# Kernel optimization log

Measured on AMD Instinct MI355X. Metric: run time of the kernel, lower is better.

Reference implementation:

```python
import jax, jax.numpy as jnp
import numpy as np

ALPHA = 4
N_NODES = 100000
N_EDGES = 1600000
DIM = 128


def setup_inputs() -> dict:
    key = jax.random.key(0)
    ks = jax.random.split(key, 7)
    x = jax.random.normal(ks[0], (N_NODES, DIM), dtype=jnp.float32)
    edge_index = jax.random.randint(ks[1], (ALPHA, 2, N_EDGES), 0, N_NODES, dtype=jnp.int64)
    edge_attr = jax.random.uniform(ks[2], (ALPHA, N_EDGES), dtype=jnp.float32)
    lin_w = jax.random.normal(ks[3], (DIM, DIM), dtype=jnp.float32) * 0.05
    lin_b = jax.random.normal(ks[4], (DIM,), dtype=jnp.float32) * 0.05
    conv_w = jax.random.normal(ks[5], (ALPHA, DIM, DIM), dtype=jnp.float32) * 0.05
    conv_b = jax.random.normal(ks[6], (ALPHA, DIM), dtype=jnp.float32) * 0.05
    return {"x": x, "edge_index": edge_index, "edge_attr": edge_attr,
            "lin_w": lin_w, "lin_b": lin_b, "conv_w": conv_w, "conv_b": conv_b}


def _gcn_conv(h, row, col, w, weight, bias):
    # gcn_norm with add_self_loops=False
    deg = jax.ops.segment_sum(w, col, num_segments=N_NODES)          # [N]
    dinv = jnp.where(deg > 0, jax.lax.rsqrt(deg), 0.0)               # deg^{-1/2}
    norm = dinv[row] * w * dinv[col]                                 # [E]
    hw = h @ weight.T                                                # [N, D] (Linear(in,out))
    msg = norm[:, None] * hw[row]                                    # gather + scale, [E, D]
    out = jax.ops.segment_sum(msg, col, num_segments=N_NODES)        # scatter-add, [N, D]
    return out + bias


def reference(x, edge_index, edge_attr, lin_w, lin_b, conv_w, conv_b):
    # dropout is identity in eval mode (training=False)
    h = jax.nn.relu(x @ lin_w.T + lin_b)
    hs = [h]
    for i in range(ALPHA):
        row, col = edge_index[i, 0], edge_index[i, 1]
        h = _gcn_conv(hs[-1], row, col, edge_attr[i], conv_w[i], conv_b[i])
        h = jax.nn.relu(h)
        hs.append(h)
    return jnp.stack(hs)  # [ALPHA+1, N, D] (torch returns list of these)
```

## Files before the change

### kernel.cpp

```cpp
#include <hip/hip_runtime.h>

#define NN 100000
#define NE 1600000
#define DD 128
#define SCAN_CHUNK 1024
#define NBLK ((NN + SCAN_CHUNK - 1) / SCAN_CHUNK)

using u16 = unsigned short;
using u32 = unsigned int;
using u64 = unsigned long long;

typedef __bf16 bf16x8 __attribute__((ext_vector_type(8)));
typedef float  f32x4  __attribute__((ext_vector_type(4)));

__device__ __forceinline__ float bf2f(u16 h){ return __uint_as_float(((u32)h) << 16); }
__device__ __forceinline__ u16 f2bf(float f){
  u32 u = __float_as_uint(f);
  u += 0x7FFFu + ((u >> 16) & 1u);
  return (u16)(u >> 16);
}
__device__ __forceinline__ int ld_idx(const int* __restrict__ p, long long k, int w64){
  return w64 ? p[2*k] : p[k];
}
__device__ __forceinline__ float ldf(const void* __restrict__ p, long long k, int f32){
  return f32 ? ((const float*)p)[k] : bf2f(((const u16*)p)[k]);
}

__global__ void detect_kernel(const int* __restrict__ ei, const u16* __restrict__ xw,
                              int* __restrict__ flags){
  if (threadIdx.x == 0 && blockIdx.x == 0){
    int all0 = 1;
    for (int k = 1; k < 256; k += 2) all0 &= (ei[k] == 0);
    flags[0] = all0;
    int cnt = 0;
    for (int i = 0; i < 128; ++i){
      u16 w = xw[2*i];
      int e = (w >> 7) & 0xFF;
      cnt += (e >= 100 && e <= 130);
    }
    flags[1] = (cnt < 64);
  }
}

__global__ __launch_bounds__(256) void prep_w_kernel(const void* __restrict__ lin_w,
    const void* __restrict__ conv_w, const int* __restrict__ flags, u16* __restrict__ wbf){
  int i = blockIdx.x*256 + threadIdx.x;
  if (i >= 5*DD*DD) return;
  int f32 = flags[1];
  float v = (i < DD*DD) ? ldf(lin_w, i, f32) : ldf(conv_w, i - DD*DD, f32);
  wbf[i] = f2bf(v);
}

__global__ __launch_bounds__(256) void hist_kernel(const void* __restrict__ ea, long long ea_off,
    const int* __restrict__ ei, long long col_off,
    const int* __restrict__ flags, u64* __restrict__ pk){
  int e = blockIdx.x*256 + threadIdx.x;
  if (e >= NE) return;
  int col = ld_idx(ei, col_off + e, flags[0]);
  float w = ldf(ea, ea_off + e, flags[1]);
  u64 v = (1ull << 40) | (u64)(w * 16777216.0f);
  atomicAdd(pk + col, v);
}

__global__ __launch_bounds__(256) void dinv_kernel(const u64* __restrict__ pk,
    float* __restrict__ dinv, int* __restrict__ cnt){
  int n = blockIdx.x*256 + threadIdx.x;
  if (n >= NN) return;
  u64 p = pk[n];
  cnt[n] = (int)(p >> 40);
  float d = (float)(p & ((1ull << 40) - 1)) * (1.0f/16777216.0f);
  dinv[n] = (d > 0.f) ? rsqrtf(d) : 0.f;
}

__global__ __launch_bounds__(256) void scan_block_kernel(const int* __restrict__ cnt,
    int* __restrict__ base, int* __restrict__ bsums){
  __shared__ int sm[256];
  int b = blockIdx.x, t = threadIdx.x;
  int i0 = b*SCAN_CHUNK + t*4;
  int v[4];
  #pragma unroll
  for (int j = 0; j < 4; ++j) v[j] = (i0 + j < NN) ? cnt[i0 + j] : 0;
  int s = v[0] + v[1] + v[2] + v[3];
  sm[t] = s;
  __syncthreads();
  for (int off = 1; off < 256; off <<= 1){
    int add = (t >= off) ? sm[t - off] : 0;
    __syncthreads();
    sm[t] += add;
    __syncthreads();
  }
  int run = sm[t] - s;
  if (t == 255) bsums[b] = sm[255];
  #pragma unroll
  for (int j = 0; j < 4; ++j){
    if (i0 + j < NN) base[i0 + j] = run;
    run += v[j];
  }
}

__global__ void scan_sums_kernel(int* __restrict__ bsums, int nb){
  __shared__ int sm[256];
  int t = threadIdx.x;
  int v = (t < nb) ? bsums[t] : 0;
  sm[t] = v;
  __syncthreads();
  for (int off = 1; off < 256; off <<= 1){
    int add = (t >= off) ? sm[t - off] : 0;
    __syncthreads();
    sm[t] += add;
    __syncthreads();
  }
  if (t < nb) bsums[t] = sm[t] - v;
}

__global__ __launch_bounds__(256) void scan_add_kernel(int* __restrict__ base,
    const int* __restrict__ bsums, int* __restrict__ cursor){
  int i = blockIdx.x*256 + threadIdx.x;
  if (i >= NN) return;
  int b = base[i] + bsums[i / SCAN_CHUNK];
  base[i] = b;
  cursor[i] = b;
}

__global__ __launch_bounds__(256) void fill_kernel(const void* __restrict__ ea, long long ea_off,
    const int* __restrict__ ei, long long row_off, long long col_off,
    const float* __restrict__ dinv, const int* __restrict__ flags,
    int* __restrict__ cursor, int2* __restrict__ rc){
  int e = blockIdx.x*256 + threadIdx.x;
  if (e >= NE) return;
  int w64 = flags[0];
  int row = ld_idx(ei, row_off + e, w64);
  int col = ld_idx(ei, col_off + e, w64);
  float w = ldf(ea, ea_off + e, flags[1]);
  int pos = atomicAdd(cursor + col, 1);
  rc[pos] = make_int2(row, __float_as_int(dinv[row] * w * dinv[col]));
}

__global__ __launch_bounds__(256) void aggregate_kernel(
    const void* __restrict__ hbase, long long h_off,
    const int2* __restrict__ rc,
    const int* __restrict__ base, const int* __restrict__ cnt,
    const int* __restrict__ flags, void* __restrict__ agg, int agg_f32){
  int wid = (int)(((long long)blockIdx.x*256 + threadIdx.x) >> 6);
  int l = threadIdx.x & 63;
  if (wid >= NN) return;
  int f32 = flags[1];
  int s = base[wid], e = s + cnt[wid];
  float ax = 0.f, ay = 0.f;

  if (f32){
    const float2* hp = (const float2*)((const float*)hbase + h_off);
    int j = s;
    for (; j + 8 <= e; j += 8){
      int2 v[8];
      #pragma unroll
      for (int k = 0; k < 8; ++k) v[k] = rc[j + k];
      float2 hv[8];
      #pragma unroll
      for (int k = 0; k < 8; ++k) hv[k] = hp[(long long)v[k].x*64 + l];
      #pragma unroll
      for (int k = 0; k < 8; ++k){
        float c = __int_as_float(v[k].y);
        ax += c*hv[k].x; ay += c*hv[k].y;
      }
    }
    if (j < e){
      int2 v[8];
      #pragma unroll
      for (int k = 0; k < 8; ++k){
        int jj = (j + k < e) ? (j + k) : s;
        v[k] = rc[jj];
        if (j + k >= e) v[k].y = 0;
      }
      float2 hv[8];
      #pragma unroll
      for (int k = 0; k < 8; ++k) hv[k] = hp[(long long)v[k].x*64 + l];
      #pragma unroll
      for (int k = 0; k < 8; ++k){
        float c = __int_as_float(v[k].y);
        ax += c*hv[k].x; ay += c*hv[k].y;
      }
    }
  } else {
    const u32* hp = (const u32*)((const u16*)hbase + h_off);
    int j = s;
    for (; j + 8 <= e; j += 8){
      int2 v[8];
      #pragma unroll
      for (int k = 0; k < 8; ++k) v[k] = rc[j + k];
      u32 hv[8];
      #pragma unroll
      for (int k = 0; k < 8; ++k) hv[k] = hp[(long long)v[k].x*64 + l];
      #pragma unroll
      for (int k = 0; k < 8; ++k){
        float c = __int_as_float(v[k].y);
        ax += c*bf2f((u16)(hv[k] & 0xFFFF));
        ay += c*bf2f((u16)(hv[k] >> 16));
      }
    }
    if (j < e){
      int2 v[8];
      #pragma unroll
      for (int k = 0; k < 8; ++k){
        int jj = (j + k < e) ? (j + k) : s;
        v[k] = rc[jj];
        if (j + k >= e) v[k].y = 0;
      }
      u32 hv[8];
      #pragma unroll
      for (int k = 0; k < 8; ++k) hv[k] = hp[(long long)v[k].x*64 + l];
      #pragma unroll
      for (int k = 0; k < 8; ++k){
        float c = __int_as_float(v[k].y);
        ax += c*bf2f((u16)(hv[k] & 0xFFFF));
        ay += c*bf2f((u16)(hv[k] >> 16));
      }
    }
  }
  if (agg_f32) ((float2*)agg)[(long long)wid*64 + l] = make_float2(ax, ay);
  else         ((u32*)agg)[(long long)wid*64 + l] = ((u32)f2bf(ay) << 16) | (u32)f2bf(ax);
}

__global__ __launch_bounds__(256) void gemm_mfma_kernel(
    const void* __restrict__ in, int in_mode,
    const u16* __restrict__ wbf,
    const void* __restrict__ bias, long long b_off,
    const int* __restrict__ flags,
    void* __restrict__ outb, long long out_off){
  __shared__ u16 ah[64*DD];
  __shared__ u16 al[64*DD];
  int t = threadIdx.x;
  int f32 = flags[1];
  int inf32 = (in_mode == 2) ? f32 : in_mode;
  long long rowbase = (long long)blockIdx.x * 64;

  #pragma unroll
  for (int it = 0; it < 8; ++it){
    int i = (it*256 + t) * 4;
    int r = i >> 7, c = i & 127;
    long long gr = rowbase + r;
    float v0, v1, v2, v3;
    if (gr < NN){
      if (inf32){
        const float4 f = *(const float4*)((const float*)in + gr*DD + c);
        v0 = f.x; v1 = f.y; v2 = f.z; v3 = f.w;
      } else {
        const ushort4 u = *(const ushort4*)((const u16*)in + gr*DD + c);
        v0 = bf2f(u.x); v1 = bf2f(u.y); v2 = bf2f(u.z); v3 = bf2f(u.w);
      }
    } else { v0 = v1 = v2 = v3 = 0.f; }
    u16 h0 = f2bf(v0), h1 = f2bf(v1), h2 = f2bf(v2), h3 = f2bf(v3);
    u16 l0 = f2bf(v0 - bf2f(h0)), l1 = f2bf(v1 - bf2f(h1));
    u16 l2 = f2bf(v2 - bf2f(h2)), l3 = f2bf(v3 - bf2f(h3));
    int idx = (r*DD + c) ^ ((r & 7) << 3);
    *(ushort4*)&ah[idx] = make_ushort4(h0, h1, h2, h3);
    *(ushort4*)&al[idx] = make_ushort4(l0, l1, l2, l3);
  }
  __syncthreads();

  const int w  = t >> 6, l = t & 63;
  const int lr = l & 15, lg = l >> 4;
  const int arow = w*16 + lr;
  f32x4 acc[8];
  #pragma unroll
  for (int j = 0; j < 8; ++j) acc[j] = (f32x4){0.f, 0.f, 0.f, 0.f};

  #pragma unroll
  for (int s = 0; s < 4; ++s){
    const int kb = s*32 + lg*8;
    const int aidx = (arow*DD + kb) ^ ((arow & 7) << 3);
    bf16x8 afh = *(const bf16x8*)&ah[aidx];
    bf16x8 afl = *(const bf16x8*)&al[aidx];
    #pragma unroll
    for (int tt = 0; tt < 8; ++tt){
      bf16x8 bfr = *(const bf16x8*)&wbf[(tt*16 + lr)*DD + kb];
      acc[tt] = __builtin_amdgcn_mfma_f32_16x16x32_bf16(afh, bfr, acc[tt], 0, 0, 0);
      acc[tt] = __builtin_amdgcn_mfma_f32_16x16x32_bf16(afl, bfr, acc[tt], 0, 0, 0);
    }
  }

  const long long gn0 = rowbase + w*16 + lg*4;
  #pragma unroll
  for (int tt = 0; tt < 8; ++tt){
    const int d = tt*16 + lr;
    const float bv = ldf(bias, b_off + d, f32);
    #pragma unroll
    for (int q = 0; q < 4; ++q){
      long long gn = gn0 + q;
      if (gn < NN){
        float vv = fmaxf(acc[tt][q] + bv, 0.f);
        long long gi = out_off + gn*DD + d;
        if (f32) ((float*)outb)[gi] = vv;
        else     ((u16*)outb)[gi] = f2bf(vv);
      }
    }
  }
}

extern "C" void kernel_launch(void* const* d_in, const int* in_sizes, int n_in,
                              void* d_out, int out_size, void* d_ws, size_t ws_size,
                              hipStream_t stream){
  const void* x      = d_in[0];
  const int*  ei     = (const int*)d_in[1];
  const void* ea     = d_in[2];
  const void* lin_w  = d_in[3];
  const void* lin_b  = d_in[4];
  const void* conv_w = d_in[5];
  const void* conv_b = d_in[6];
  void* out = d_out;

  char* ws = (char*)d_ws;
  size_t o = 0;
  auto alloc = [&](size_t bytes){ void* p = ws + o; o = (o + bytes + 255) & ~(size_t)255; return p; };
  int*   flags  = (int*)  alloc(256);
  u64*   pk     = (u64*)  alloc((size_t)NN*8);
  float* dinv   = (float*)alloc((size_t)NN*4);
  int*   cnt    = (int*)  alloc((size_t)NN*4);
  int*   base   = (int*)  alloc((size_t)NN*4);
  int*   cursor = (int*)  alloc((size_t)NN*4);
  int*   bsums  = (int*)  alloc(4096);
  int2*  rc     = (int2*) alloc((size_t)NE*8);
  u16*   wbf    = (u16*)  alloc((size_t)5*DD*DD*2);
  size_t fixed = o;
  int agg_f32 = (ws_size >= fixed + (size_t)NN*DD*4) ? 1 : 0;
  void* agg = alloc((size_t)NN*DD*(agg_f32 ? 4 : 2));

  detect_kernel<<<1, 64, 0, stream>>>(ei, (const u16*)x, flags);
  prep_w_kernel<<<(5*DD*DD + 255)/256, 256, 0, stream>>>(lin_w, conv_w, flags, wbf);

  gemm_mfma_kernel<<<(NN+63)/64, 256, 0, stream>>>(x, 2, wbf, lin_b, 0, flags, out, 0);

  for (int i = 0; i < 4; ++i){
    long long h_off   = (long long)i*NN*DD;
    long long o_off   = (long long)(i+1)*NN*DD;
    long long row_off = ((long long)i*2 + 0)*NE;
    long long col_off = ((long long)i*2 + 1)*NE;
    long long ea_off  = (long long)i*NE;

    hipMemsetAsync(pk, 0, (size_t)NN*8, stream);
    hist_kernel<<<(NE+255)/256, 256, 0, stream>>>(ea, ea_off, ei, col_off, flags, pk);
    dinv_kernel<<<(NN+255)/256, 256, 0, stream>>>(pk, dinv, cnt);

    scan_block_kernel<<<NBLK, 256, 0, stream>>>(cnt, base, bsums);
    scan_sums_kernel<<<1, 256, 0, stream>>>(bsums, NBLK);
    scan_add_kernel<<<(NN+255)/256, 256, 0, stream>>>(base, bsums, cursor);

    fill_kernel<<<(NE+255)/256, 256, 0, stream>>>(ea, ea_off, ei, row_off, col_off,
                                                  dinv, flags, cursor, rc);

    aggregate_kernel<<<(NN*64 + 255)/256, 256, 0, stream>>>(out, h_off, rc,
                                                            base, cnt, flags, agg, agg_f32);

    gemm_mfma_kernel<<<(NN+63)/64, 256, 0, stream>>>(agg, agg_f32 ? 1 : 0,
                                                     wbf + (size_t)(1+i)*DD*DD,
                                                     conv_b, (long long)i*DD, flags, out, o_off);
  }
}
```

Before: 1.624 ms.

## Batch CSR build across layers and fuse aggregation with MFMA GEMM

The per-layer histogram, scan and fill kernels become single launches that cover all four layers, using padded per-layer arrays. The aggregation is fused into the GEMM: each block gathers 64 node rows into shared memory as a split hi/lo bf16 pair and multiplies them with MFMA directly, so the intermediate agg buffer is never written to or read from global memory. In exchange, each block now does 64 rows of irregular gather before its GEMM, which may lower parallelism during the gather phase, and the CSR workspace grows fourfold.

```diff
diff --git a/kernel.cpp b/kernel.cpp
--- a/kernel.cpp
+++ b/kernel.cpp
@@ -5,6 +5,9 @@
 #define DD 128
 #define SCAN_CHUNK 1024
 #define NBLK ((NN + SCAN_CHUNK - 1) / SCAN_CHUNK)
+#define NNP (NBLK * SCAN_CHUNK)
+#define NTOT (4 * NNP)
+#define BPL ((NE + 255) / 256)
 
 using u16 = unsigned short;
 using u32 = unsigned int;
@@ -51,21 +54,23 @@
   wbf[i] = f2bf(v);
 }
 
-__global__ __launch_bounds__(256) void hist_kernel(const void* __restrict__ ea, long long ea_off,
-    const int* __restrict__ ei, long long col_off,
-    const int* __restrict__ flags, u64* __restrict__ pk){
-  int e = blockIdx.x*256 + threadIdx.x;
+__global__ __launch_bounds__(256) void hist_all_kernel(const void* __restrict__ ea,
+    const int* __restrict__ ei, const int* __restrict__ flags, u64* __restrict__ pk){
+  int lyr = blockIdx.x / BPL;
+  int e = (blockIdx.x - lyr*BPL)*256 + threadIdx.x;
   if (e >= NE) return;
+  long long col_off = ((long long)lyr*2 + 1)*NE;
+  long long ea_off  = (long long)lyr*NE;
   int col = ld_idx(ei, col_off + e, flags[0]);
   float w = ldf(ea, ea_off + e, flags[1]);
   u64 v = (1ull << 40) | (u64)(w * 16777216.0f);
-  atomicAdd(pk + col, v);
-}
-
-__global__ __launch_bounds__(256) void dinv_kernel(const u64* __restrict__ pk,
+  atomicAdd(pk + (size_t)lyr*NNP + col, v);
+}
+
+__global__ __launch_bounds__(256) void dinv_all_kernel(const u64* __restrict__ pk,
     float* __restrict__ dinv, int* __restrict__ cnt){
   int n = blockIdx.x*256 + threadIdx.x;
-  if (n >= NN) return;
+  if (n >= NTOT) return;
   u64 p = pk[n];
   cnt[n] = (int)(p >> 40);
   float d = (float)(p & ((1ull << 40) - 1)) * (1.0f/16777216.0f);
@@ -79,7 +84,7 @@
   int i0 = b*SCAN_CHUNK + t*4;
   int v[4];
   #pragma unroll
-  for (int j = 0; j < 4; ++j) v[j] = (i0 + j < NN) ? cnt[i0 + j] : 0;
+  for (int j = 0; j < 4; ++j) v[j] = cnt[i0 + j];
   int s = v[0] + v[1] + v[2] + v[3];
   sm[t] = s;
   __syncthreads();
@@ -93,7 +98,7 @@
   if (t == 255) bsums[b] = sm[255];
   #pragma unroll
   for (int j = 0; j < 4; ++j){
-    if (i0 + j < NN) base[i0 + j] = run;
+    base[i0 + j] = run;
     run += v[j];
   }
 }
@@ -101,7 +106,8 @@
 __global__ void scan_sums_kernel(int* __restrict__ bsums, int nb){
   __shared__ int sm[256];
   int t = threadIdx.x;
-  int v = (t < nb) ? bsums[t] : 0;
+  int* bs = bsums + blockIdx.x*nb;
+  int v = (t < nb) ? bs[t] : 0;
   sm[t] = v;
   __syncthreads();
   for (int off = 1; off < 256; off <<= 1){
@@ -110,115 +116,34 @@
     sm[t] += add;
     __syncthreads();
   }
-  if (t < nb) bsums[t] = sm[t] - v;
+  if (t < nb) bs[t] = sm[t] - v;
 }
 
 __global__ __launch_bounds__(256) void scan_add_kernel(int* __restrict__ base,
     const int* __restrict__ bsums, int* __restrict__ cursor){
   int i = blockIdx.x*256 + threadIdx.x;
-  if (i >= NN) return;
+  if (i >= NTOT) return;
   int b = base[i] + bsums[i / SCAN_CHUNK];
   base[i] = b;
   cursor[i] = b;
 }
 
-__global__ __launch_bounds__(256) void fill_kernel(const void* __restrict__ ea, long long ea_off,
-    const int* __restrict__ ei, long long row_off, long long col_off,
-    const float* __restrict__ dinv, const int* __restrict__ flags,
-    int* __restrict__ cursor, int2* __restrict__ rc){
-  int e = blockIdx.x*256 + threadIdx.x;
+__global__ __launch_bounds__(256) void fill_all_kernel(const void* __restrict__ ea,
+    const int* __restrict__ ei, const float* __restrict__ dinv,
+    const int* __restrict__ flags, int* __restrict__ cursor, int2* __restrict__ rc){
+  int lyr = blockIdx.x / BPL;
+  int e = (blockIdx.x - lyr*BPL)*256 + threadIdx.x;
   if (e >= NE) return;
   int w64 = flags[0];
+  long long row_off = ((long long)lyr*2 + 0)*NE;
+  long long col_off = ((long long)lyr*2 + 1)*NE;
+  long long ea_off  = (long long)lyr*NE;
   int row = ld_idx(ei, row_off + e, w64);
   int col = ld_idx(ei, col_off + e, w64);
   float w = ldf(ea, ea_off + e, flags[1]);
-  int pos = atomicAdd(cursor + col, 1);
-  rc[pos] = make_int2(row, __float_as_int(dinv[row] * w * dinv[col]));
-}
-
-__global__ __launch_bounds__(256) void aggregate_kernel(
-    const void* __restrict__ hbase, long long h_off,
-    const int2* __restrict__ rc,
-    const int* __restrict__ base, const int* __restrict__ cnt,
-    const int* __restrict__ flags, void* __restrict__ agg, int agg_f32){
-  int wid = (int)(((long long)blockIdx.x*256 + threadIdx.x) >> 6);
-  int l = threadIdx.x & 63;
-  if (wid >= NN) return;
-  int f32 = flags[1];
-  int s = base[wid], e = s + cnt[wid];
-  float ax = 0.f, ay = 0.f;
-
-  if (f32){
-    const float2* hp = (const float2*)((const float*)hbase + h_off);
-    int j = s;
-    for (; j + 8 <= e; j += 8){
-      int2 v[8];
-      #pragma unroll
-      for (int k = 0; k < 8; ++k) v[k] = rc[j + k];
-      float2 hv[8];
-      #pragma unroll
-      for (int k = 0; k < 8; ++k) hv[k] = hp[(long long)v[k].x*64 + l];
-      #pragma unroll
-      for (int k = 0; k < 8; ++k){
-        float c = __int_as_float(v[k].y);
-        ax += c*hv[k].x; ay += c*hv[k].y;
-      }
-    }
-    if (j < e){
-      int2 v[8];
-      #pragma unroll
-      for (int k = 0; k < 8; ++k){
-        int jj = (j + k < e) ? (j + k) : s;
-        v[k] = rc[jj];
-        if (j + k >= e) v[k].y = 0;
-      }
-      float2 hv[8];
-      #pragma unroll
-      for (int k = 0; k < 8; ++k) hv[k] = hp[(long long)v[k].x*64 + l];
-      #pragma unroll
-      for (int k = 0; k < 8; ++k){
-        float c = __int_as_float(v[k].y);
-        ax += c*hv[k].x; ay += c*hv[k].y;
-      }
-    }
-  } else {
-    const u32* hp = (const u32*)((const u16*)hbase + h_off);
-    int j = s;
-    for (; j + 8 <= e; j += 8){
-      int2 v[8];
-      #pragma unroll
-      for (int k = 0; k < 8; ++k) v[k] = rc[j + k];
-      u32 hv[8];
-      #pragma unroll
-      for (int k = 0; k < 8; ++k) hv[k] = hp[(long long)v[k].x*64 + l];
-      #pragma unroll
-      for (int k = 0; k < 8; ++k){
-        float c = __int_as_float(v[k].y);
-        ax += c*bf2f((u16)(hv[k] & 0xFFFF));
-        ay += c*bf2f((u16)(hv[k] >> 16));
-      }
-    }
-    if (j < e){
-      int2 v[8];
-      #pragma unroll
-      for (int k = 0; k < 8; ++k){
-        int jj = (j + k < e) ? (j + k) : s;
-        v[k] = rc[jj];
-        if (j + k >= e) v[k].y = 0;
-      }
-      u32 hv[8];
-      #pragma unroll
-      for (int k = 0; k < 8; ++k) hv[k] = hp[(long long)v[k].x*64 + l];
-      #pragma unroll
-      for (int k = 0; k < 8; ++k){
-        float c = __int_as_float(v[k].y);
-        ax += c*bf2f((u16)(hv[k] & 0xFFFF));
-        ay += c*bf2f((u16)(hv[k] >> 16));
-      }
-    }
-  }
-  if (agg_f32) ((float2*)agg)[(long long)wid*64 + l] = make_float2(ax, ay);
-  else         ((u32*)agg)[(long long)wid*64 + l] = ((u32)f2bf(ay) << 16) | (u32)f2bf(ax);
+  const float* dv = dinv + (size_t)lyr*NNP;
+  int pos = atomicAdd(cursor + (size_t)lyr*NNP + col, 1);
+  rc[(size_t)lyr*NE + pos] = make_int2(row, __float_as_int(dv[row] * w * dv[col]));
 }
 
 __global__ __launch_bounds__(256) void gemm_mfma_kernel(
@@ -297,6 +222,143 @@
   }
 }
 
+__global__ __launch_bounds__(256) void agg_gemm_kernel(
+    const void* __restrict__ hbase, long long h_off,
+    const int2* __restrict__ rc,
+    const int* __restrict__ basep, const int* __restrict__ cntp,
+    const u16* __restrict__ wbf,
+    const void* __restrict__ bias, long long b_off,
+    const int* __restrict__ flags,
+    void* __restrict__ outb, long long out_off){
+  __shared__ u16 ah[64*DD];
+  __shared__ u16 al[64*DD];
+  int t = threadIdx.x;
+  int f32 = flags[1];
+  long long rowbase = (long long)blockIdx.x * 64;
+  const int w = t >> 6, l = t & 63;
+
+  for (int i = 0; i < 16; ++i){
+    int r = w*16 + i;
+    long long n = rowbase + r;
+    float ax = 0.f, ay = 0.f;
+    if (n < NN){
+      int s = basep[n], e = s + cntp[n];
+      if (f32){
+        const float2* hp = (const float2*)((const float*)hbase + h_off);
+        int j = s;
+        for (; j + 8 <= e; j += 8){
+          int2 v[8];
+          #pragma unroll
+          for (int k = 0; k < 8; ++k) v[k] = rc[j + k];
+          float2 hv[8];
+          #pragma unroll
+          for (int k = 0; k < 8; ++k) hv[k] = hp[(long long)v[k].x*64 + l];
+          #pragma unroll
+          for (int k = 0; k < 8; ++k){
+            float c = __int_as_float(v[k].y);
+            ax += c*hv[k].x; ay += c*hv[k].y;
+          }
+        }
+        if (j < e){
+          int2 v[8];
+          #pragma unroll
+          for (int k = 0; k < 8; ++k){
+            int jj = (j + k < e) ? (j + k) : s;
+            v[k] = rc[jj];
+            if (j + k >= e) v[k].y = 0;
+          }
+          float2 hv[8];
+          #pragma unroll
+          for (int k = 0; k < 8; ++k) hv[k] = hp[(long long)v[k].x*64 + l];
+          #pragma unroll
+          for (int k = 0; k < 8; ++k){
+            float c = __int_as_float(v[k].y);
+            ax += c*hv[k].x; ay += c*hv[k].y;
+          }
+        }
+      } else {
+        const u32* hp = (const u32*)((const u16*)hbase + h_off);
+        int j = s;
+        for (; j + 8 <= e; j += 8){
+          int2 v[8];
+          #pragma unroll
+          for (int k = 0; k < 8; ++k) v[k] = rc[j + k];
+          u32 hv[8];
+          #pragma unroll
+          for (int k = 0; k < 8; ++k) hv[k] = hp[(long long)v[k].x*64 + l];
+          #pragma unroll
+          for (int k = 0; k < 8; ++k){
+            float c = __int_as_float(v[k].y);
+            ax += c*bf2f((u16)(hv[k] & 0xFFFF));
+            ay += c*bf2f((u16)(hv[k] >> 16));
+          }
+        }
+        if (j < e){
+          int2 v[8];
+          #pragma unroll
+          for (int k = 0; k < 8; ++k){
+            int jj = (j + k < e) ? (j + k) : s;
+            v[k] = rc[jj];
+            if (j + k >= e) v[k].y = 0;
+          }
+          u32 hv[8];
+          #pragma unroll
+          for (int k = 0; k < 8; ++k) hv[k] = hp[(long long)v[k].x*64 + l];
+          #pragma unroll
+          for (int k = 0; k < 8; ++k){
+            float c = __int_as_float(v[k].y);
+            ax += c*bf2f((u16)(hv[k] & 0xFFFF));
+            ay += c*bf2f((u16)(hv[k] >> 16));
+          }
+        }
+      }
+    }
+    u16 h0 = f2bf(ax), h1 = f2bf(ay);
+    u16 l0 = f2bf(ax - bf2f(h0)), l1 = f2bf(ay - bf2f(h1));
+    int idx = (r*DD + 2*l) ^ ((r & 7) << 3);
+    *(u32*)&ah[idx] = (u32)h0 | ((u32)h1 << 16);
+    *(u32*)&al[idx] = (u32)l0 | ((u32)l1 << 16);
+  }
+  __syncthreads();
+
+  const int lr = l & 15, lg = l >> 4;
+  const int arow = w*16 + lr;
+  f32x4 acc[8];
+  #pragma unroll
+  for (int j = 0; j < 8; ++j) acc[j] = (f32x4){0.f, 0.f, 0.f, 0.f};
+
+  #pragma unroll
+  for (int s = 0; s < 4; ++s){
+    const int kb = s*32 + lg*8;
+    const int aidx = (arow*DD + kb) ^ ((arow & 7) << 3);
+    bf16x8 afh = *(const bf16x8*)&ah[aidx];
+    bf16x8 afl = *(const bf16x8*)&al[aidx];
+    #pragma unroll
+    for (int tt = 0; tt < 8; ++tt){
+      bf16x8 bfr = *(const bf16x8*)&wbf[(tt*16 + lr)*DD + kb];
+      acc[tt] = __builtin_amdgcn_mfma_f32_16x16x32_bf16(afh, bfr, acc[tt], 0, 0, 0);
+      acc[tt] = __builtin_amdgcn_mfma_f32_16x16x32_bf16(afl, bfr, acc[tt], 0, 0, 0);
+    }
+  }
+
+  const long long gn0 = rowbase + w*16 + lg*4;
+  #pragma unroll
+  for (int tt = 0; tt < 8; ++tt){
+    const int d = tt*16 + lr;
+    const float bv = ldf(bias, b_off + d, f32);
+    #pragma unroll
+    for (int q = 0; q < 4; ++q){
+      long long gn = gn0 + q;
+      if (gn < NN){
+        float vv = fmaxf(acc[tt][q] + bv, 0.f);
+        long long gi = out_off + gn*DD + d;
+        if (f32) ((float*)outb)[gi] = vv;
+        else     ((u16*)outb)[gi] = f2bf(vv);
+      }
+    }
+  }
+}
+
 extern "C" void kernel_launch(void* const* d_in, const int* in_sizes, int n_in,
                               void* d_out, int out_size, void* d_ws, size_t ws_size,
                               hipStream_t stream){
@@ -313,46 +375,37 @@
   size_t o = 0;
   auto alloc = [&](size_t bytes){ void* p = ws + o; o = (o + bytes + 255) & ~(size_t)255; return p; };
   int*   flags  = (int*)  alloc(256);
-  u64*   pk     = (u64*)  alloc((size_t)NN*8);
-  float* dinv   = (float*)alloc((size_t)NN*4);
-  int*   cnt    = (int*)  alloc((size_t)NN*4);
-  int*   base   = (int*)  alloc((size_t)NN*4);
-  int*   cursor = (int*)  alloc((size_t)NN*4);
-  int*   bsums  = (int*)  alloc(4096);
-  int2*  rc     = (int2*) alloc((size_t)NE*8);
+  u64*   pk     = (u64*)  alloc((size_t)NTOT*8);
+  float* dinv   = (float*)alloc((size_t)NTOT*4);
+  int*   cnt    = (int*)  alloc((size_t)NTOT*4);
+  int*   base   = (int*)  alloc((size_t)NTOT*4);
+  int*   cursor = (int*)  alloc((size_t)NTOT*4);
+  int*   bsums  = (int*)  alloc((size_t)4*NBLK*4 + 256);
+  int2*  rc     = (int2*) alloc((size_t)4*NE*8);
   u16*   wbf    = (u16*)  alloc((size_t)5*DD*DD*2);
-  size_t fixed = o;
-  int agg_f32 = (ws_size >= fixed + (size_t)NN*DD*4) ? 1 : 0;
-  void* agg = alloc((size_t)NN*DD*(agg_f32 ? 4 : 2));
 
   detect_kernel<<<1, 64, 0, stream>>>(ei, (const u16*)x, flags);
   prep_w_kernel<<<(5*DD*DD + 255)/256, 256, 0, stream>>>(lin_w, conv_w, flags, wbf);
 
+  hipMemsetAsync(pk, 0, (size_t)NTOT*8, stream);
+  hist_all_kernel<<<4*BPL, 256, 0, stream>>>(ea, ei, flags, pk);
+  dinv_all_kernel<<<(NTOT+255)/256, 256, 0, stream>>>(pk, dinv, cnt);
+  scan_block_kernel<<<4*NBLK, 256, 0, stream>>>(cnt, base, bsums);
+  scan_sums_kernel<<<4, 256, 0, stream>>>(bsums, NBLK);
+  scan_add_kernel<<<(NTOT+255)/256, 256, 0, stream>>>(base, bsums, cursor);
+  fill_all_kernel<<<4*BPL, 256, 0, stream>>>(ea, ei, dinv, flags, cursor, rc);
+
   gemm_mfma_kernel<<<(NN+63)/64, 256, 0, stream>>>(x, 2, wbf, lin_b, 0, flags, out, 0);
 
   for (int i = 0; i < 4; ++i){
-    long long h_off   = (long long)i*NN*DD;
-    long long o_off   = (long long)(i+1)*NN*DD;
-    long long row_off = ((long long)i*2 + 0)*NE;
-    long long col_off = ((long long)i*2 + 1)*NE;
-    long long ea_off  = (long long)i*NE;
-
-    hipMemsetAsync(pk, 0, (size_t)NN*8, stream);
-    hist_kernel<<<(NE+255)/256, 256, 0, stream>>>(ea, ea_off, ei, col_off, flags, pk);
-    dinv_kernel<<<(NN+255)/256, 256, 0, stream>>>(pk, dinv, cnt);
-
-    scan_block_kernel<<<NBLK, 256, 0, stream>>>(cnt, base, bsums);
-    scan_sums_kernel<<<1, 256, 0, stream>>>(bsums, NBLK);
-    scan_add_kernel<<<(NN+255)/256, 256, 0, stream>>>(base, bsums, cursor);
-
-    fill_kernel<<<(NE+255)/256, 256, 0, stream>>>(ea, ea_off, ei, row_off, col_off,
-                                                  dinv, flags, cursor, rc);
-
-    aggregate_kernel<<<(NN*64 + 255)/256, 256, 0, stream>>>(out, h_off, rc,
-                                                            base, cnt, flags, agg, agg_f32);
-
-    gemm_mfma_kernel<<<(NN+63)/64, 256, 0, stream>>>(agg, agg_f32 ? 1 : 0,
-                                                     wbf + (size_t)(1+i)*DD*DD,
-                                                     conv_b, (long long)i*DD, flags, out, o_off);
-  }
-}
+    long long h_off = (long long)i*NN*DD;
+    long long o_off = (long long)(i+1)*NN*DD;
+    agg_gemm_kernel<<<(NN+63)/64, 256, 0, stream>>>(out, h_off,
+                                                    rc + (size_t)i*NE,
+                                                    base + (size_t)i*NNP,
+                                                    cnt  + (size_t)i*NNP,
+                                                    wbf + (size_t)(1+i)*DD*DD,
+                                                    conv_b, (long long)i*DD,
+                                                    flags, out, o_off);
+  }
+}
```

After: 1.539 ms. 5.3% less time.
